# Performance work log

Measured on AMD Instinct MI355X. Metric: run time of the kernel, lower is better.

Reference implementation:

```python
import jax, jax.numpy as jnp
import numpy as np

N = 100000      # num nodes
E = 1600000     # num edges (avg degree 16)
F_IN = 256      # num_node_features
HID = 128       # hid_dim
C = 16          # num_classes


def gcn_conv(x, W, b, src, dst, num_nodes):
    # Linear transform first (PyG GCNConv transforms then aggregates)
    h = x @ W  # [N, out]
    # Symmetric normalization with self-loops already included in src/dst
    ones = jnp.ones_like(dst, dtype=h.dtype)
    deg = jax.ops.segment_sum(ones, dst, num_segments=num_nodes)  # in-degree incl. self-loop
    dinv = jnp.where(deg > 0, jax.lax.rsqrt(deg), 0.0)
    norm = dinv[src] * dinv[dst]                 # [E+N]
    msg = h[src] * norm[:, None]                 # gather + scale
    out = jax.ops.segment_sum(msg, dst, num_segments=num_nodes)  # scatter-add
    return out + b


def setup_inputs() -> dict:
    key = jax.random.key(0)
    k = jax.random.split(key, 4)
    x = jax.random.normal(k[0], (N, F_IN), dtype=jnp.float32)
    edge_index = jax.random.randint(k[1], (2, E), 0, N, dtype=jnp.int32)
    W1 = jax.random.normal(k[2], (F_IN, HID), dtype=jnp.float32) * (1.0 / np.sqrt(F_IN))
    b1 = jnp.zeros((HID,), dtype=jnp.float32)
    W2 = jax.random.normal(k[3], (HID, C), dtype=jnp.float32) * (1.0 / np.sqrt(HID))
    b2 = jnp.zeros((C,), dtype=jnp.float32)
    return {"x": x, "edge_index": edge_index, "W1": W1, "b1": b1, "W2": W2, "b2": b2}


def reference(x, edge_index, W1, b1, W2, b2):
    num_nodes = x.shape[0]
    loop = jnp.arange(num_nodes, dtype=edge_index.dtype)
    src = jnp.concatenate([edge_index[0], loop])  # add self-loops
    dst = jnp.concatenate([edge_index[1], loop])
    h = gcn_conv(x, W1, b1, src, dst, num_nodes)
    h = jax.nn.relu(h)
    # F.dropout(training=self.training): identity in eval mode
    out = gcn_conv(h, W2, b2, src, dst, num_nodes)
    return out
```

## Files before the change

kernel.cpp:

```cpp
#include <hip/hip_runtime.h>
#include <cstddef>

#define CAP 48

typedef short short8 __attribute__((ext_vector_type(8)));
typedef float floatx4 __attribute__((ext_vector_type(4)));

__device__ inline float b2f(unsigned short u) {
  union { unsigned int i; float f; } c;
  c.i = ((unsigned int)u) << 16;
  return c.f;
}
__device__ inline float b2f_lo(unsigned int u) {
  union { unsigned int i; float f; } c;
  c.i = u << 16;
  return c.f;
}
__device__ inline float b2f_hi(unsigned int u) {
  union { unsigned int i; float f; } c;
  c.i = u & 0xFFFF0000u;
  return c.f;
}
__device__ inline unsigned short f2b(float f) {
  union { float f; unsigned int i; } c;
  c.f = f;
  unsigned int u = c.i;
  unsigned int r = (u + 0x7FFFu + ((u >> 16) & 1u)) >> 16;
  return (unsigned short)r;
}

__global__ void k_zero(int* __restrict__ cnt, int N) {
  int i = blockIdx.x * blockDim.x + threadIdx.x;
  if (i < N) cnt[i] = 0;
}

__global__ __launch_bounds__(256) void k_build(const int* __restrict__ src,
                                               const int* __restrict__ dst,
                                               int E, int N,
                                               int* __restrict__ cnt,
                                               int* __restrict__ bucket) {
  const int g = blockIdx.x & 7;
  const int S = (N + 7) >> 3;
  const int lo = g * S;
  const int hi = min(N, lo + S);
  const int tb = (blockIdx.x >> 3) * 256 + (int)threadIdx.x;
  const int T = (gridDim.x >> 3) * 256;
  const int E4 = E & ~3;

  for (int i0 = tb * 4; i0 < E4; i0 += T * 4) {
    int4 d4 = *(const int4*)(dst + i0);
    int4 s4 = *(const int4*)(src + i0);
    int p0 = CAP, p1 = CAP, p2 = CAP, p3 = CAP;
    if (d4.x >= lo && d4.x < hi) p0 = atomicAdd(&cnt[d4.x], 1);
    if (d4.y >= lo && d4.y < hi) p1 = atomicAdd(&cnt[d4.y], 1);
    if (d4.z >= lo && d4.z < hi) p2 = atomicAdd(&cnt[d4.z], 1);
    if (d4.w >= lo && d4.w < hi) p3 = atomicAdd(&cnt[d4.w], 1);
    if (p0 < CAP) bucket[(size_t)d4.x * CAP + p0] = s4.x;
    if (p1 < CAP) bucket[(size_t)d4.y * CAP + p1] = s4.y;
    if (p2 < CAP) bucket[(size_t)d4.z * CAP + p2] = s4.z;
    if (p3 < CAP) bucket[(size_t)d4.w * CAP + p3] = s4.w;
  }
  if (tb < E - E4) {
    int i = E4 + tb;
    int d = dst[i], s = src[i];
    if (d >= lo && d < hi) {
      int pos = atomicAdd(&cnt[d], 1);
      if (pos < CAP) bucket[(size_t)d * CAP + pos] = s;
    }
  }
}

__global__ void k_dinv(const int* __restrict__ cnt, float* __restrict__ dinv, int N) {
  int i = blockIdx.x * blockDim.x + threadIdx.x;
  if (i < N) dinv[i] = rsqrtf((float)(cnt[i] + 1));
}

__global__ void k_w1t(const float* __restrict__ W1, unsigned short* __restrict__ W1T) {
  int i = blockIdx.x * 256 + threadIdx.x;
  int k = i >> 7, n = i & 127;
  W1T[n * 256 + k] = f2b(W1[i]);
}

__global__ __launch_bounds__(256) void k_gemm1(const float* __restrict__ X,
                                               const unsigned short* __restrict__ W1T,
                                               unsigned short* __restrict__ H1, int M) {
  __shared__ unsigned short As[64 * 72];
  __shared__ unsigned short Bs[128 * 72];
  const int tid = threadIdx.x;
  const int wave = tid >> 6;
  const int lane = tid & 63;
  const int quad = lane >> 4;
  const int l16 = lane & 15;
  const int row0 = blockIdx.x * 64;
  const int n0 = wave * 32;

  floatx4 acc[4][2];
#pragma unroll
  for (int r = 0; r < 4; r++)
#pragma unroll
    for (int c = 0; c < 2; c++) acc[r][c] = (floatx4){0.f, 0.f, 0.f, 0.f};

  for (int k0 = 0; k0 < 256; k0 += 64) {
    {
      int r = tid >> 2;
      int qk = (tid & 3) * 16;
      int gr = row0 + r;
      float4 v[4];
#pragma unroll
      for (int u = 0; u < 4; u++) v[u] = make_float4(0.f, 0.f, 0.f, 0.f);
      if (gr < M) {
        const float4* xp = (const float4*)(X + (size_t)gr * 256 + k0 + qk);
#pragma unroll
        for (int u = 0; u < 4; u++) v[u] = xp[u];
      }
      unsigned short tmp[16];
#pragma unroll
      for (int u = 0; u < 4; u++) {
        tmp[u * 4 + 0] = f2b(v[u].x); tmp[u * 4 + 1] = f2b(v[u].y);
        tmp[u * 4 + 2] = f2b(v[u].z); tmp[u * 4 + 3] = f2b(v[u].w);
      }
      unsigned short* p = As + r * 72 + qk;
      *(uint4*)(p) = *(const uint4*)(tmp);
      *(uint4*)(p + 8) = *(const uint4*)(tmp + 8);
    }
    {
      int n = tid >> 1;
      int half = (tid & 1) * 32;
      const uint4* wp = (const uint4*)(W1T + (size_t)n * 256 + k0 + half);
      uint4 w0 = wp[0];
      uint4 w1 = wp[1];
      uint4 w2 = wp[2];
      uint4 w3 = wp[3];
      unsigned short* p = Bs + n * 72 + half;
      *(uint4*)(p) = w0;
      *(uint4*)(p + 8) = w1;
      *(uint4*)(p + 16) = w2;
      *(uint4*)(p + 24) = w3;
    }
    __syncthreads();

#pragma unroll
    for (int s = 0; s < 2; s++) {
      short8 afr[4], bfr[2];
#pragma unroll
      for (int r = 0; r < 4; r++)
        afr[r] = *(const short8*)(As + (r * 16 + l16) * 72 + s * 32 + quad * 8);
#pragma unroll
      for (int c = 0; c < 2; c++)
        bfr[c] = *(const short8*)(Bs + (n0 + c * 16 + l16) * 72 + s * 32 + quad * 8);
#pragma unroll
      for (int r = 0; r < 4; r++)
#pragma unroll
        for (int c = 0; c < 2; c++)
          acc[r][c] = __builtin_amdgcn_mfma_f32_16x16x32_bf16(afr[r], bfr[c], acc[r][c], 0, 0, 0);
    }
    __syncthreads();
  }

#pragma unroll
  for (int r = 0; r < 4; r++) {
#pragma unroll
    for (int c = 0; c < 2; c++) {
      int col = n0 + c * 16 + l16;
#pragma unroll
      for (int i = 0; i < 4; i++) {
        int gr = row0 + r * 16 + quad * 4 + i;
        if (gr < M) H1[(size_t)gr * 128 + col] = f2b(acc[r][c][i]);
      }
    }
  }
}

__global__ __launch_bounds__(256) void k_agg1(const unsigned short* __restrict__ H1,
                                              const int* __restrict__ cnt,
                                              const int* __restrict__ bucket,
                                              const float* __restrict__ dinv,
                                              const float* __restrict__ b1,
                                              unsigned short* __restrict__ A1, int N) {
  const int lane = threadIdx.x & 15;
  const int node = blockIdx.x * 16 + (threadIdx.x >> 4);
  if (node >= N) return;
  const float di = dinv[node];
  const float wself = di * di;
  const int deg = min(cnt[node], CAP);
  const int* bk = bucket + (size_t)node * CAP;

  int idx0 = (lane < deg) ? bk[lane] : 0;
  int idx1 = (lane + 16 < deg) ? bk[lane + 16] : 0;
  int idx2 = (lane + 32 < deg) ? bk[lane + 32] : 0;
  float dv0 = (lane < deg) ? dinv[idx0] : 0.f;
  float dv1 = (lane + 16 < deg) ? dinv[idx1] : 0.f;
  float dv2 = (lane + 32 < deg) ? dinv[idx2] : 0.f;

  uint4 hs = ((const uint4*)(H1 + (size_t)node * 128))[lane];
  float a0 = b2f_lo(hs.x) * wself, a1 = b2f_hi(hs.x) * wself;
  float a2 = b2f_lo(hs.y) * wself, a3 = b2f_hi(hs.y) * wself;
  float a4 = b2f_lo(hs.z) * wself, a5 = b2f_hi(hs.z) * wself;
  float a6 = b2f_lo(hs.w) * wself, a7 = b2f_hi(hs.w) * wself;
  float c0 = 0.f, c1 = 0.f, c2 = 0.f, c3 = 0.f, c4 = 0.f, c5 = 0.f, c6 = 0.f, c7 = 0.f;

  for (int j = 0; j < deg; j += 4) {
    int b = j >> 4;
    int idxB = (b == 0) ? idx0 : ((b == 1) ? idx1 : idx2);
    float dvB = (b == 0) ? dv0 : ((b == 1) ? dv1 : dv2);
    int base = j & 15;
    int s0 = __shfl(idxB, base + 0, 16);
    int s1 = __shfl(idxB, base + 1, 16);
    int s2 = __shfl(idxB, base + 2, 16);
    int s3 = __shfl(idxB, base + 3, 16);
    float w0 = __shfl(dvB, base + 0, 16) * di;
    float w1 = __shfl(dvB, base + 1, 16) * di;
    float w2 = __shfl(dvB, base + 2, 16) * di;
    float w3 = __shfl(dvB, base + 3, 16) * di;
    uint4 v0 = ((const uint4*)(H1 + (size_t)s0 * 128))[lane];
    uint4 v1 = ((const uint4*)(H1 + (size_t)s1 * 128))[lane];
    uint4 v2 = ((const uint4*)(H1 + (size_t)s2 * 128))[lane];
    uint4 v3 = ((const uint4*)(H1 + (size_t)s3 * 128))[lane];
    a0 += b2f_lo(v0.x) * w0; a1 += b2f_hi(v0.x) * w0;
    a2 += b2f_lo(v0.y) * w0; a3 += b2f_hi(v0.y) * w0;
    a4 += b2f_lo(v0.z) * w0; a5 += b2f_hi(v0.z) * w0;
    a6 += b2f_lo(v0.w) * w0; a7 += b2f_hi(v0.w) * w0;
    c0 += b2f_lo(v1.x) * w1; c1 += b2f_hi(v1.x) * w1;
    c2 += b2f_lo(v1.y) * w1; c3 += b2f_hi(v1.y) * w1;
    c4 += b2f_lo(v1.z) * w1; c5 += b2f_hi(v1.z) * w1;
    c6 += b2f_lo(v1.w) * w1; c7 += b2f_hi(v1.w) * w1;
    a0 += b2f_lo(v2.x) * w2; a1 += b2f_hi(v2.x) * w2;
    a2 += b2f_lo(v2.y) * w2; a3 += b2f_hi(v2.y) * w2;
    a4 += b2f_lo(v2.z) * w2; a5 += b2f_hi(v2.z) * w2;
    a6 += b2f_lo(v2.w) * w2; a7 += b2f_hi(v2.w) * w2;
    c0 += b2f_lo(v3.x) * w3; c1 += b2f_hi(v3.x) * w3;
    c2 += b2f_lo(v3.y) * w3; c3 += b2f_hi(v3.y) * w3;
    c4 += b2f_lo(v3.z) * w3; c5 += b2f_hi(v3.z) * w3;
    c6 += b2f_lo(v3.w) * w3; c7 += b2f_hi(v3.w) * w3;
  }
  a0 += c0; a1 += c1; a2 += c2; a3 += c3;
  a4 += c4; a5 += c5; a6 += c6; a7 += c7;

  float4 bb0 = ((const float4*)b1)[lane * 2];
  float4 bb1 = ((const float4*)b1)[lane * 2 + 1];
  a0 = fmaxf(a0 + bb0.x, 0.f); a1 = fmaxf(a1 + bb0.y, 0.f);
  a2 = fmaxf(a2 + bb0.z, 0.f); a3 = fmaxf(a3 + bb0.w, 0.f);
  a4 = fmaxf(a4 + bb1.x, 0.f); a5 = fmaxf(a5 + bb1.y, 0.f);
  a6 = fmaxf(a6 + bb1.z, 0.f); a7 = fmaxf(a7 + bb1.w, 0.f);
  uint4 o;
  o.x = (unsigned int)f2b(a0) | ((unsigned int)f2b(a1) << 16);
  o.y = (unsigned int)f2b(a2) | ((unsigned int)f2b(a3) << 16);
  o.z = (unsigned int)f2b(a4) | ((unsigned int)f2b(a5) << 16);
  o.w = (unsigned int)f2b(a6) | ((unsigned int)f2b(a7) << 16);
  ((uint4*)(A1 + (size_t)node * 128))[lane] = o;
}

__global__ __launch_bounds__(256) void k_gemm2(const unsigned short* __restrict__ A1,
                                               const float* __restrict__ W2,
                                               unsigned short* __restrict__ H2, int M) {
  __shared__ float Ws[128 * 16];
  int tid = threadIdx.x;
  ((float4*)Ws)[tid] = ((const float4*)W2)[tid];
  ((float4*)Ws)[tid + 256] = ((const float4*)W2)[tid + 256];
  __syncthreads();
  int q = tid & 3;
  int row = blockIdx.x * 64 + (tid >> 2);
  if (row >= M) return;
  float4 acc = make_float4(0.f, 0.f, 0.f, 0.f);
  const unsigned short* arow = A1 + (size_t)row * 128;
  for (int k0 = 0; k0 < 128; k0 += 8) {
    uint4 av = *(const uint4*)(arow + k0);
    float a[8];
    a[0] = b2f_lo(av.x); a[1] = b2f_hi(av.x);
    a[2] = b2f_lo(av.y); a[3] = b2f_hi(av.y);
    a[4] = b2f_lo(av.z); a[5] = b2f_hi(av.z);
    a[6] = b2f_lo(av.w); a[7] = b2f_hi(av.w);
#pragma unroll
    for (int kk = 0; kk < 8; kk++) {
      float4 wv = *(const float4*)&Ws[(k0 + kk) * 16 + q * 4];
      acc.x += a[kk] * wv.x; acc.y += a[kk] * wv.y;
      acc.z += a[kk] * wv.z; acc.w += a[kk] * wv.w;
    }
  }
  ushort4 o;
  o.x = f2b(acc.x); o.y = f2b(acc.y); o.z = f2b(acc.z); o.w = f2b(acc.w);
  ((ushort4*)(H2 + (size_t)row * 16))[q] = o;
}

__global__ __launch_bounds__(256) void k_agg2(const unsigned short* __restrict__ H2,
                                              const int* __restrict__ cnt,
                                              const int* __restrict__ bucket,
                                              const float* __restrict__ dinv,
                                              const float* __restrict__ b2,
                                              float* __restrict__ out, int N) {
  const int half = threadIdx.x & 1;
  const int node = blockIdx.x * 128 + (threadIdx.x >> 1);
  if (node >= N) return;
  const float di = dinv[node];
  const float wself = di * di;
  const int deg = min(cnt[node], CAP);
  const int* bk = bucket + (size_t)node * CAP;

  uint4 h = ((const uint4*)(H2 + (size_t)node * 16))[half];
  float a0 = b2f_lo(h.x) * wself, a1 = b2f_hi(h.x) * wself;
  float a2 = b2f_lo(h.y) * wself, a3 = b2f_hi(h.y) * wself;
  float a4 = b2f_lo(h.z) * wself, a5 = b2f_hi(h.z) * wself;
  float a6 = b2f_lo(h.w) * wself, a7 = b2f_hi(h.w) * wself;

  for (int j = 0; j < deg; j += 4) {
    int4 s4 = *(const int4*)(bk + j);
    int s0 = s4.x;
    int s1 = (j + 1 < deg) ? s4.y : 0;
    int s2 = (j + 2 < deg) ? s4.z : 0;
    int s3 = (j + 3 < deg) ? s4.w : 0;
    float w0 = dinv[s0] * di;
    float w1 = (j + 1 < deg) ? dinv[s1] * di : 0.f;
    float w2 = (j + 2 < deg) ? dinv[s2] * di : 0.f;
    float w3 = (j + 3 < deg) ? dinv[s3] * di : 0.f;
    uint4 v0 = ((const uint4*)(H2 + (size_t)s0 * 16))[half];
    uint4 v1 = ((const uint4*)(H2 + (size_t)s1 * 16))[half];
    uint4 v2 = ((const uint4*)(H2 + (size_t)s2 * 16))[half];
    uint4 v3 = ((const uint4*)(H2 + (size_t)s3 * 16))[half];
    a0 += b2f_lo(v0.x) * w0 + b2f_lo(v1.x) * w1 + b2f_lo(v2.x) * w2 + b2f_lo(v3.x) * w3;
    a1 += b2f_hi(v0.x) * w0 + b2f_hi(v1.x) * w1 + b2f_hi(v2.x) * w2 + b2f_hi(v3.x) * w3;
    a2 += b2f_lo(v0.y) * w0 + b2f_lo(v1.y) * w1 + b2f_lo(v2.y) * w2 + b2f_lo(v3.y) * w3;
    a3 += b2f_hi(v0.y) * w0 + b2f_hi(v1.y) * w1 + b2f_hi(v2.y) * w2 + b2f_hi(v3.y) * w3;
    a4 += b2f_lo(v0.z) * w0 + b2f_lo(v1.z) * w1 + b2f_lo(v2.z) * w2 + b2f_lo(v3.z) * w3;
    a5 += b2f_hi(v0.z) * w0 + b2f_hi(v1.z) * w1 + b2f_hi(v2.z) * w2 + b2f_hi(v3.z) * w3;
    a6 += b2f_lo(v0.w) * w0 + b2f_lo(v1.w) * w1 + b2f_lo(v2.w) * w2 + b2f_lo(v3.w) * w3;
    a7 += b2f_hi(v0.w) * w0 + b2f_hi(v1.w) * w1 + b2f_hi(v2.w) * w2 + b2f_hi(v3.w) * w3;
  }

  float4 bb0 = ((const float4*)b2)[half * 2];
  float4 bb1 = ((const float4*)b2)[half * 2 + 1];
  float4 o0 = make_float4(a0 + bb0.x, a1 + bb0.y, a2 + bb0.z, a3 + bb0.w);
  float4 o1 = make_float4(a4 + bb1.x, a5 + bb1.y, a6 + bb1.z, a7 + bb1.w);
  ((float4*)(out + (size_t)node * 16))[half * 2] = o0;
  ((float4*)(out + (size_t)node * 16))[half * 2 + 1] = o1;
}


extern "C" void kernel_launch(void* const* d_in, const int* in_sizes, int n_in,
                              void* d_out, int out_size, void* d_ws, size_t ws_size,
                              hipStream_t stream) {
  const float* x  = (const float*)d_in[0];
  const int* eidx = (const int*)d_in[1];
  const float* W1 = (const float*)d_in[2];
  const float* b1 = (const float*)d_in[3];
  const float* W2 = (const float*)d_in[4];
  const float* b2 = (const float*)d_in[5];
  float* out = (float*)d_out;

  const int HID = in_sizes[3];
  const int F   = in_sizes[2] / HID;
  const int N   = in_sizes[0] / F;
  const int E   = in_sizes[1] / 2;
  (void)n_in; (void)out_size; (void)ws_size;

  const int* src = eidx;
  const int* dst = eidx + E;

  char* base = (char*)d_ws;
  size_t off = 0;
  auto alloc = [&](size_t bytes) -> char* {
    char* p = base + off;
    off = (off + bytes + 255) & ~(size_t)255;
    return p;
  };
  int*            cnt    = (int*)alloc((size_t)N * 4);
  float*          dinv   = (float*)alloc((size_t)N * 4);
  int*            bucket = (int*)alloc((size_t)N * CAP * 4);
  unsigned short* w1t    = (unsigned short*)alloc((size_t)256 * 128 * 2);
  unsigned short* h1     = (unsigned short*)alloc((size_t)N * 128 * 2);
  unsigned short* a1     = (unsigned short*)alloc((size_t)N * 128 * 2);
  unsigned short* h2     = (unsigned short*)alloc((size_t)N * 16 * 2);

  const int nbN = (N + 255) / 256;

  hipLaunchKernelGGL(k_zero, dim3(nbN), dim3(256), 0, stream, cnt, N);
  hipLaunchKernelGGL(k_build, dim3(8 * 512), dim3(256), 0, stream, src, dst, E, N, cnt, bucket);
  hipLaunchKernelGGL(k_dinv, dim3(nbN), dim3(256), 0, stream, cnt, dinv, N);
  hipLaunchKernelGGL(k_w1t, dim3(128), dim3(256), 0, stream, W1, w1t);
  hipLaunchKernelGGL(k_gemm1, dim3((N + 63) / 64), dim3(256), 0, stream, x, w1t, h1, N);
  hipLaunchKernelGGL(k_agg1, dim3((N + 15) / 16), dim3(256), 0, stream, h1, cnt, bucket,
                     dinv, b1, a1, N);
  hipLaunchKernelGGL(k_gemm2, dim3((N + 63) / 64), dim3(256), 0, stream, a1, W2, h2, N);
  hipLaunchKernelGGL(k_agg2, dim3((N + 127) / 128), dim3(256), 0, stream, h2, cnt, bucket,
                     dinv, b2, out, N);
}
```

Measured before the change: 355.1 us.

## Fuse graph build with GEMM1 in one launch and compute dinv on the fly

```diff
diff --git a/kernel.cpp b/kernel.cpp
--- a/kernel.cpp
+++ b/kernel.cpp
@@ -2,15 +2,11 @@
 #include <cstddef>
 
 #define CAP 48
+#define NBUILD 4096
 
 typedef short short8 __attribute__((ext_vector_type(8)));
 typedef float floatx4 __attribute__((ext_vector_type(4)));
 
-__device__ inline float b2f(unsigned short u) {
-  union { unsigned int i; float f; } c;
-  c.i = ((unsigned int)u) << 16;
-  return c.f;
-}
 __device__ inline float b2f_lo(unsigned int u) {
   union { unsigned int i; float f; } c;
   c.i = u << 16;
@@ -28,70 +24,66 @@
   unsigned int r = (u + 0x7FFFu + ((u >> 16) & 1u)) >> 16;
   return (unsigned short)r;
 }
-
-__global__ void k_zero(int* __restrict__ cnt, int N) {
-  int i = blockIdx.x * blockDim.x + threadIdx.x;
+__device__ inline float dinv_of(int c) { return rsqrtf((float)(c + 1)); }
+
+__global__ void k_prep(int* __restrict__ cnt, int N,
+                       const float* __restrict__ W1, unsigned short* __restrict__ W1T) {
+  int i = blockIdx.x * 256 + threadIdx.x;
   if (i < N) cnt[i] = 0;
-}
-
-__global__ __launch_bounds__(256) void k_build(const int* __restrict__ src,
-                                               const int* __restrict__ dst,
-                                               int E, int N,
-                                               int* __restrict__ cnt,
-                                               int* __restrict__ bucket) {
-  const int g = blockIdx.x & 7;
-  const int S = (N + 7) >> 3;
-  const int lo = g * S;
-  const int hi = min(N, lo + S);
-  const int tb = (blockIdx.x >> 3) * 256 + (int)threadIdx.x;
-  const int T = (gridDim.x >> 3) * 256;
-  const int E4 = E & ~3;
-
-  for (int i0 = tb * 4; i0 < E4; i0 += T * 4) {
-    int4 d4 = *(const int4*)(dst + i0);
-    int4 s4 = *(const int4*)(src + i0);
-    int p0 = CAP, p1 = CAP, p2 = CAP, p3 = CAP;
-    if (d4.x >= lo && d4.x < hi) p0 = atomicAdd(&cnt[d4.x], 1);
-    if (d4.y >= lo && d4.y < hi) p1 = atomicAdd(&cnt[d4.y], 1);
-    if (d4.z >= lo && d4.z < hi) p2 = atomicAdd(&cnt[d4.z], 1);
-    if (d4.w >= lo && d4.w < hi) p3 = atomicAdd(&cnt[d4.w], 1);
-    if (p0 < CAP) bucket[(size_t)d4.x * CAP + p0] = s4.x;
-    if (p1 < CAP) bucket[(size_t)d4.y * CAP + p1] = s4.y;
-    if (p2 < CAP) bucket[(size_t)d4.z * CAP + p2] = s4.z;
-    if (p3 < CAP) bucket[(size_t)d4.w * CAP + p3] = s4.w;
-  }
-  if (tb < E - E4) {
-    int i = E4 + tb;
-    int d = dst[i], s = src[i];
-    if (d >= lo && d < hi) {
-      int pos = atomicAdd(&cnt[d], 1);
-      if (pos < CAP) bucket[(size_t)d * CAP + pos] = s;
-    }
-  }
-}
-
-__global__ void k_dinv(const int* __restrict__ cnt, float* __restrict__ dinv, int N) {
-  int i = blockIdx.x * blockDim.x + threadIdx.x;
-  if (i < N) dinv[i] = rsqrtf((float)(cnt[i] + 1));
-}
-
-__global__ void k_w1t(const float* __restrict__ W1, unsigned short* __restrict__ W1T) {
-  int i = blockIdx.x * 256 + threadIdx.x;
-  int k = i >> 7, n = i & 127;
-  W1T[n * 256 + k] = f2b(W1[i]);
-}
-
-__global__ __launch_bounds__(256) void k_gemm1(const float* __restrict__ X,
-                                               const unsigned short* __restrict__ W1T,
-                                               unsigned short* __restrict__ H1, int M) {
+  if (i < 256 * 128) {
+    int k = i >> 7, n = i & 127;
+    W1T[n * 256 + k] = f2b(W1[i]);
+  }
+}
+
+__global__ __launch_bounds__(256) void k_build_gemm1(
+    const int* __restrict__ src, const int* __restrict__ dst, int E, int N,
+    int* __restrict__ cnt, int* __restrict__ bucket,
+    const float* __restrict__ X, const unsigned short* __restrict__ W1T,
+    unsigned short* __restrict__ H1, int M) {
   __shared__ unsigned short As[64 * 72];
   __shared__ unsigned short Bs[128 * 72];
+
+  if ((int)blockIdx.x < NBUILD) {
+    const int g = blockIdx.x & 7;
+    const int S = (N + 7) >> 3;
+    const int lo = g * S;
+    const int hi = min(N, lo + S);
+    const int tb = ((int)blockIdx.x >> 3) * 256 + (int)threadIdx.x;
+    const int T = (NBUILD >> 3) * 256;
+    const int E4 = E & ~3;
+
+    for (int i0 = tb * 4; i0 < E4; i0 += T * 4) {
+      int4 d4 = *(const int4*)(dst + i0);
+      int4 s4 = *(const int4*)(src + i0);
+      int p0 = CAP, p1 = CAP, p2 = CAP, p3 = CAP;
+      if (d4.x >= lo && d4.x < hi) p0 = atomicAdd(&cnt[d4.x], 1);
+      if (d4.y >= lo && d4.y < hi) p1 = atomicAdd(&cnt[d4.y], 1);
+      if (d4.z >= lo && d4.z < hi) p2 = atomicAdd(&cnt[d4.z], 1);
+      if (d4.w >= lo && d4.w < hi) p3 = atomicAdd(&cnt[d4.w], 1);
+      if (p0 < CAP) bucket[(size_t)d4.x * CAP + p0] = s4.x;
+      if (p1 < CAP) bucket[(size_t)d4.y * CAP + p1] = s4.y;
+      if (p2 < CAP) bucket[(size_t)d4.z * CAP + p2] = s4.z;
+      if (p3 < CAP) bucket[(size_t)d4.w * CAP + p3] = s4.w;
+    }
+    if (tb < E - E4) {
+      int i = E4 + tb;
+      int d = dst[i], s = src[i];
+      if (d >= lo && d < hi) {
+        int pos = atomicAdd(&cnt[d], 1);
+        if (pos < CAP) bucket[(size_t)d * CAP + pos] = s;
+      }
+    }
+    return;
+  }
+
+  const int bid = (int)blockIdx.x - NBUILD;
   const int tid = threadIdx.x;
   const int wave = tid >> 6;
   const int lane = tid & 63;
   const int quad = lane >> 4;
   const int l16 = lane & 15;
-  const int row0 = blockIdx.x * 64;
+  const int row0 = bid * 64;
   const int n0 = wave * 32;
 
   floatx4 acc[4][2];
@@ -174,23 +166,23 @@
 __global__ __launch_bounds__(256) void k_agg1(const unsigned short* __restrict__ H1,
                                               const int* __restrict__ cnt,
                                               const int* __restrict__ bucket,
-                                              const float* __restrict__ dinv,
                                               const float* __restrict__ b1,
                                               unsigned short* __restrict__ A1, int N) {
   const int lane = threadIdx.x & 15;
   const int node = blockIdx.x * 16 + (threadIdx.x >> 4);
   if (node >= N) return;
-  const float di = dinv[node];
+  const int cn = cnt[node];
+  const float di = dinv_of(cn);
   const float wself = di * di;
-  const int deg = min(cnt[node], CAP);
+  const int deg = min(cn, CAP);
   const int* bk = bucket + (size_t)node * CAP;
 
   int idx0 = (lane < deg) ? bk[lane] : 0;
   int idx1 = (lane + 16 < deg) ? bk[lane + 16] : 0;
   int idx2 = (lane + 32 < deg) ? bk[lane + 32] : 0;
-  float dv0 = (lane < deg) ? dinv[idx0] : 0.f;
-  float dv1 = (lane + 16 < deg) ? dinv[idx1] : 0.f;
-  float dv2 = (lane + 32 < deg) ? dinv[idx2] : 0.f;
+  float dv0 = (lane < deg) ? dinv_of(cnt[idx0]) : 0.f;
+  float dv1 = (lane + 16 < deg) ? dinv_of(cnt[idx1]) : 0.f;
+  float dv2 = (lane + 32 < deg) ? dinv_of(cnt[idx2]) : 0.f;
 
   uint4 hs = ((const uint4*)(H1 + (size_t)node * 128))[lane];
   float a0 = b2f_lo(hs.x) * wself, a1 = b2f_hi(hs.x) * wself;
@@ -285,15 +277,15 @@
 __global__ __launch_bounds__(256) void k_agg2(const unsigned short* __restrict__ H2,
                                               const int* __restrict__ cnt,
                                               const int* __restrict__ bucket,
-                                              const float* __restrict__ dinv,
                                               const float* __restrict__ b2,
                                               float* __restrict__ out, int N) {
   const int half = threadIdx.x & 1;
   const int node = blockIdx.x * 128 + (threadIdx.x >> 1);
   if (node >= N) return;
-  const float di = dinv[node];
+  const int cn = cnt[node];
+  const float di = dinv_of(cn);
   const float wself = di * di;
-  const int deg = min(cnt[node], CAP);
+  const int deg = min(cn, CAP);
   const int* bk = bucket + (size_t)node * CAP;
 
   uint4 h = ((const uint4*)(H2 + (size_t)node * 16))[half];
@@ -308,10 +300,10 @@
     int s1 = (j + 1 < deg) ? s4.y : 0;
     int s2 = (j + 2 < deg) ? s4.z : 0;
     int s3 = (j + 3 < deg) ? s4.w : 0;
-    float w0 = dinv[s0] * di;
-    float w1 = (j + 1 < deg) ? dinv[s1] * di : 0.f;
-    float w2 = (j + 2 < deg) ? dinv[s2] * di : 0.f;
-    float w3 = (j + 3 < deg) ? dinv[s3] * di : 0.f;
+    float w0 = dinv_of(cnt[s0]) * di;
+    float w1 = (j + 1 < deg) ? dinv_of(cnt[s1]) * di : 0.f;
+    float w2 = (j + 2 < deg) ? dinv_of(cnt[s2]) * di : 0.f;
+    float w3 = (j + 3 < deg) ? dinv_of(cnt[s3]) * di : 0.f;
     uint4 v0 = ((const uint4*)(H2 + (size_t)s0 * 16))[half];
     uint4 v1 = ((const uint4*)(H2 + (size_t)s1 * 16))[half];
     uint4 v2 = ((const uint4*)(H2 + (size_t)s2 * 16))[half];
@@ -363,7 +355,6 @@
     return p;
   };
   int*            cnt    = (int*)alloc((size_t)N * 4);
-  float*          dinv   = (float*)alloc((size_t)N * 4);
   int*            bucket = (int*)alloc((size_t)N * CAP * 4);
   unsigned short* w1t    = (unsigned short*)alloc((size_t)256 * 128 * 2);
   unsigned short* h1     = (unsigned short*)alloc((size_t)N * 128 * 2);
@@ -371,15 +362,14 @@
   unsigned short* h2     = (unsigned short*)alloc((size_t)N * 16 * 2);
 
   const int nbN = (N + 255) / 256;
-
-  hipLaunchKernelGGL(k_zero, dim3(nbN), dim3(256), 0, stream, cnt, N);
-  hipLaunchKernelGGL(k_build, dim3(8 * 512), dim3(256), 0, stream, src, dst, E, N, cnt, bucket);
-  hipLaunchKernelGGL(k_dinv, dim3(nbN), dim3(256), 0, stream, cnt, dinv, N);
-  hipLaunchKernelGGL(k_w1t, dim3(128), dim3(256), 0, stream, W1, w1t);
-  hipLaunchKernelGGL(k_gemm1, dim3((N + 63) / 64), dim3(256), 0, stream, x, w1t, h1, N);
+  const int gblocks = (N + 63) / 64;
+
+  hipLaunchKernelGGL(k_prep, dim3(nbN), dim3(256), 0, stream, cnt, N, W1, w1t);
+  hipLaunchKernelGGL(k_build_gemm1, dim3(NBUILD + gblocks), dim3(256), 0, stream,
+                     src, dst, E, N, cnt, bucket, x, w1t, h1, N);
   hipLaunchKernelGGL(k_agg1, dim3((N + 15) / 16), dim3(256), 0, stream, h1, cnt, bucket,
-                     dinv, b1, a1, N);
+                     b1, a1, N);
   hipLaunchKernelGGL(k_gemm2, dim3((N + 63) / 64), dim3(256), 0, stream, a1, W2, h2, N);
   hipLaunchKernelGGL(k_agg2, dim3((N + 127) / 128), dim3(256), 0, stream, h2, cnt, bucket,
-                     dinv, b2, out, N);
-}
+                     b2, out, N);
+}
```

Result: faster. 345.4 us (-2.7%).
